# Kernel optimization log

Measured on AMD Instinct MI355X. Metric: run time of the kernel, lower is better.

The kernel has to match this reference:

```python
import jax, jax.numpy as jnp
import numpy as np

EMBED_DIM = 2048
NUM_HEADS = 16
HEAD_DIM = EMBED_DIM // NUM_HEADS
BATCH, SEQ = 4, 4096


def setup_inputs() -> dict:
    key = jax.random.key(0)
    k1, k2, k3, k4 = jax.random.split(key, 4)
    scale = 1.0 / np.sqrt(EMBED_DIM)
    x = jax.random.normal(k1, (BATCH, SEQ, EMBED_DIM), dtype=jnp.float32)
    W_qkv = jax.random.normal(k2, (EMBED_DIM, 3 * EMBED_DIM), dtype=jnp.float32) * scale
    W_out = jax.random.normal(k3, (EMBED_DIM, EMBED_DIM), dtype=jnp.float32) * scale
    b_out = jax.random.normal(k4, (EMBED_DIM,), dtype=jnp.float32) * 0.01
    return {"x": x, "W_qkv": W_qkv, "W_out": W_out, "b_out": b_out}


def reference(x, W_qkv, W_out, b_out):
    b, s, _ = x.shape
    # qkv: (b, s, 3, h, d)
    qkv = (x @ W_qkv).reshape(b, s, 3, NUM_HEADS, HEAD_DIM)
    q, k, v = qkv[:, :, 0], qkv[:, :, 1], qkv[:, :, 2]
    # NOTE: faithful to source — scores mix HEADS per token: (b, s, h, h)
    scores = jnp.einsum('bshd,bsHd->bshH', q, k) / jnp.sqrt(jnp.float32(HEAD_DIM))
    w = jax.nn.softmax(scores, axis=-1)
    attn = jnp.einsum('bshH,bsHd->bshd', w, v).reshape(b, s, EMBED_DIM)
    return attn @ W_out + b_out
```

## Files before the change

kernel.cpp:

```cpp
#include <hip/hip_runtime.h>
#include <hip/hip_bf16.h>
#include <cstdint>


#define TOKENS 16384
#define EMB    2048
#define NQKV   6144

typedef __bf16 bf16x8_t __attribute__((ext_vector_type(8)));
typedef float  f32x4_t  __attribute__((ext_vector_type(4)));

#define GLOAD16(gsrc, ldst)                                                    \
  __builtin_amdgcn_global_load_lds(                                            \
      (const __attribute__((address_space(1))) void*)(uintptr_t)(gsrc),        \
      (__attribute__((address_space(3))) void*)(uint32_t)(uintptr_t)(ldst),    \
      16, 0, 0)

static __device__ __forceinline__ unsigned short f32_to_bf16_bits(float f) {
  union { float f; uint32_t u; } x; x.f = f;
  uint32_t u = x.u;
  u += 0x7fffu + ((u >> 16) & 1u);
  return (unsigned short)(u >> 16);
}

__global__ __launch_bounds__(256) void prep(
    const float4* __restrict__ x4, ushort4* __restrict__ xb4,
    const float* __restrict__ Wqkv, unsigned short* __restrict__ wqkvT,
    const float* __restrict__ Wout, unsigned short* __restrict__ woutT) {
  const int b = blockIdx.x;
  const int t = threadIdx.x;
  if (b < 2048) {
    const int n4 = 33554432 / 4;
    const int stride = 2048 * 256;
    for (int i = b * 256 + t; i < n4; i += stride) {
      float4 v = x4[i];
      ushort4 o;
      o.x = f32_to_bf16_bits(v.x);
      o.y = f32_to_bf16_bits(v.y);
      o.z = f32_to_bf16_bits(v.z);
      o.w = f32_to_bf16_bits(v.w);
      xb4[i] = o;
    }
    return;
  }
  __shared__ float tile[32][33];
  const float* in;
  unsigned short* out;
  int R, C, bxt, byt;
  if (b < 14336) {
    const int bb = b - 2048;
    in = Wqkv; out = wqkvT; R = 2048; C = 6144;
    bxt = bb % 192; byt = bb / 192;
  } else {
    const int bb = b - 14336;
    in = Wout; out = woutT; R = 2048; C = 2048;
    bxt = bb % 64; byt = bb / 64;
  }
  const int bx = bxt * 32;
  const int by = byt * 32;
  const int tx = t & 31;
  const int ty = t >> 5;
#pragma unroll
  for (int j = 0; j < 32; j += 8)
    tile[ty + j][tx] = in[(size_t)(by + ty + j) * C + bx + tx];
  __syncthreads();
#pragma unroll
  for (int j = 0; j < 32; j += 8)
    out[(size_t)(bx + ty + j) * R + by + tx] = f32_to_bf16_bits(tile[tx][ty + j]);
}

template <bool OUT_BF16>
__global__ __launch_bounds__(512, 1) void gemm_bt(
    const unsigned short* __restrict__ A,
    const unsigned short* __restrict__ BT,
    unsigned short* __restrict__ Cb,
    float* __restrict__ Cf,
    const float* __restrict__ bias,
    int M, int N) {
  constexpr int K = 2048;
  constexpr int BK = 64;
  constexpr int NKT = K / BK;
  __shared__ __align__(16) char lds[131072];

  const int nbx = N / 256;
  const int nwg = gridDim.x;
  const int bid = blockIdx.x;
  const int swzb = (bid & 7) * (nwg >> 3) + (bid >> 3);
  const int by = swzb / nbx;
  const int bx = swzb % nbx;

  const int t    = threadIdx.x;
  const int lane = t & 63;
  const int wid  = t >> 6;
  const int wr   = wid >> 2;
  const int wc   = wid & 3;
  const int lr   = lane & 15;
  const int g    = lane >> 4;
  const bool g0  = (wr == 0);

  const unsigned short* aSrc = A  + (size_t)by * 256 * K;
  const unsigned short* bSrc = BT + (size_t)bx * 256 * K;

  int aoff[2], boff[2];
#pragma unroll
  for (int i = 0; i < 2; ++i) {
    const int p   = (i * 512 + t) * 16;
    const int lo  = p ^ (((p >> 7) & 7) << 4);
    const int rih = lo >> 7;
    const int kbe = (lo & 127) >> 1;
    aoff[i] = (((rih >> 6) << 7) + (rih & 63)) * K + kbe;
    boff[i] = (((rih >> 5) << 6) + (rih & 31)) * K + kbe;
  }
  const int ldst = wid << 10;

  auto stageA = [&](int h, int k0, char* bufA) {
#pragma unroll
    for (int i = 0; i < 2; ++i)
      GLOAD16(aSrc + aoff[i] + h * (64 * K) + k0, bufA + h * 16384 + i * 8192 + ldst);
  };
  auto stageB = [&](int h, int k0, char* bufB) {
#pragma unroll
    for (int i = 0; i < 2; ++i)
      GLOAD16(bSrc + boff[i] + h * (32 * K) + k0, bufB + h * 16384 + i * 8192 + ldst);
  };

  const int sw   = (lr & 7) << 4;
  const int col0 = (g * 16) ^ sw;
  const int col1 = (64 + g * 16) ^ sw;
  const int aRow = (wr * 64 + lr) * 128;
  const int bRow = (wc * 32 + lr) * 128;

  f32x4_t acc[8][4] = {};
  bf16x8_t av[4][2];
  bf16x8_t bv0[2][2], bv1[2][2];

#define LDA_INTO(dst, bufA_, q)                                                \
  {                                                                            \
    const char* _b = (bufA_) + (q) * 16384 + aRow;                             \
    _Pragma("unroll") for (int m2 = 0; m2 < 4; ++m2) {                         \
      dst[m2][0] = *(const bf16x8_t*)(_b + m2 * 2048 + col0);                  \
      dst[m2][1] = *(const bf16x8_t*)(_b + m2 * 2048 + col1);                  \
    }                                                                          \
  }
#define LDB_INTO(dst, bufB_, pair)                                             \
  {                                                                            \
    _Pragma("unroll") for (int e = 0; e < 2; ++e) {                            \
      const int nf = (pair) * 2 + e;                                           \
      const char* _b = (bufB_) + (nf >> 1) * 16384 + (nf & 1) * 2048 + bRow;   \
      dst[e][0] = *(const bf16x8_t*)(_b + col0);                               \
      dst[e][1] = *(const bf16x8_t*)(_b + col1);                               \
    }                                                                          \
  }
#define MFMAQ(AV, BV, Q, PAIR)                                                 \
  _Pragma("unroll") for (int m2 = 0; m2 < 4; ++m2)                             \
  _Pragma("unroll") for (int e = 0; e < 2; ++e)                                \
  _Pragma("unroll") for (int ks = 0; ks < 2; ++ks)                             \
    acc[(Q) * 4 + m2][(PAIR) * 2 + e] = __builtin_amdgcn_mfma_f32_16x16x32_bf16( \
        AV[m2][ks], BV[e][ks], acc[(Q) * 4 + m2][(PAIR) * 2 + e], 0, 0, 0);

#define SBR __builtin_amdgcn_sched_barrier(0)
#define BARR __builtin_amdgcn_s_barrier()
#define LGKM0 asm volatile("s_waitcnt lgkmcnt(0)" ::: "memory"); SBR;
#define P1_ __builtin_amdgcn_s_setprio(1);
#define P0_ __builtin_amdgcn_s_setprio(0); SBR;

#define MQ0 { LGKM0; P1_; MFMAQ(av, bv0, 0, 0); MFMAQ(av, bv1, 0, 1); P0_; }
#define MQ1 { LGKM0; P1_; MFMAQ(av, bv0, 1, 0); MFMAQ(av, bv1, 1, 1); P0_; }

#define BODY(KT, SA1, SB2, VMN, MP)                                            \
  {                                                                            \
    char* cA = lds + ((KT) & 1) * 65536;                                       \
    char* cB = cA + 32768;                                                     \
    char* nA = lds + (((KT) + 1) & 1) * 65536;                                 \
    const int k1 = ((KT) + 1) * BK, k2 = ((KT) + 2) * BK;                      \
               \
    if (g0) { LDA_INTO(av, cA, 0); LDB_INTO(bv0, cB, 0); LDB_INTO(bv1, cB, 1); } \
    SBR;                                                                       \
    if (SA1) { stageA(0, k1, nA); } SBR;                                       \
    if (!g0 && (MP)) MQ1;                                                      \
    SBR; BARR;                                                                 \
                        \
    if (!g0) { LDA_INTO(av, cA, 0); LDB_INTO(bv0, cB, 0); LDB_INTO(bv1, cB, 1); } \
    SBR;                                                                       \
    if (SA1) { stageA(1, k1, nA); } SBR;                                       \
    if (g0) MQ0;                                                               \
    SBR; BARR;                                                                 \
                                         \
    if (g0) { LDA_INTO(av, cA, 1); } SBR;                                      \
    if (!g0) MQ0;                                                              \
    SBR; BARR;                                                                 \
                   \
    if (!g0) { LDA_INTO(av, cA, 1); } SBR;                                     \
    if (SB2) { stageB(0, k2, cB); stageB(1, k2, cB); } SBR;                    \
    asm volatile("s_waitcnt vmcnt(" #VMN ")" ::: "memory"); SBR;               \
    if (g0) MQ1;                                                               \
    SBR; BARR;                                                                 \
  }

  {
    char* b0A = lds;
    char* b0B = lds + 32768;
    char* b1B = lds + 65536 + 32768;
    stageB(0, 0, b0B); stageB(1, 0, b0B);
    stageA(0, 0, b0A);
    stageA(1, 0, b0A);
    stageB(0, BK, b1B); stageB(1, BK, b1B);
    asm volatile("s_waitcnt vmcnt(4)" ::: "memory");
    BARR;
  }

  BODY(0, 1, 1, 4, 0);
  for (int kt = 1; kt < NKT - 2; ++kt) {
    BODY(kt, 1, 1, 4, 1);
  }
  BODY(NKT - 2, 1, 0, 0, 1);
  BODY(NKT - 1, 0, 0, 0, 1);
  if (!g0) MQ1;

  const int rbase = by * 256 + wr * 128 + g * 4;
  const int cbase = bx * 256 + wc * 64 + lr;
#pragma unroll
  for (int m = 0; m < 8; ++m) {
#pragma unroll
    for (int nf = 0; nf < 4; ++nf) {
      const int col = cbase + nf * 16;
#pragma unroll
      for (int j = 0; j < 4; ++j) {
        const size_t off = (size_t)(rbase + (m >> 2) * 64 + (m & 3) * 16 + j) * N + col;
        if constexpr (OUT_BF16) {
          Cb[off] = f32_to_bf16_bits(acc[m][nf][j]);
        } else {
          Cf[off] = acc[m][nf][j] + bias[col];
        }
      }
    }
  }
#undef LDA_INTO
#undef LDB_INTO
#undef MFMAQ
#undef SBR
#undef BARR
#undef LGKM0
#undef P1_
#undef P0_
#undef MQ0
#undef MQ1
#undef BODY
}

__global__ __launch_bounds__(256) void attn_heads(
    const unsigned short* __restrict__ qkv,
    unsigned short* __restrict__ attn) {
  __shared__ __align__(16) unsigned short sQKV[NQKV];
  __shared__ float sW[16][16];

  const int t = threadIdx.x;
  const size_t qbase = (size_t)blockIdx.x * NQKV;

  const uint4* gp = (const uint4*)(qkv + qbase);
  uint4* l = (uint4*)sQKV;
#pragma unroll
  for (int i = 0; i < 3; ++i) {
    const int idx = i * 256 + t;
    int dst = idx;
    if (idx >= 256 && idx < 512) {
      const int r = (idx - 256) >> 4;
      const int c = idx & 15;
      dst = 256 + r * 16 + (c ^ (r & 7));
    }
    l[dst] = gp[idx];
  }
  __syncthreads();

  const int h = t >> 4;
  const int H = t & 15;
  const bf16x8_t* q8 = (const bf16x8_t*)sQKV + h * 16;
  const bf16x8_t* k8 = (const bf16x8_t*)sQKV + 256;
  float s = 0.f;
#pragma unroll
  for (int d8 = 0; d8 < 16; ++d8) {
    bf16x8_t qv = q8[d8];
    bf16x8_t kv = k8[H * 16 + (d8 ^ (H & 7))];
#pragma unroll
    for (int j = 0; j < 8; ++j)
      s = fmaf((float)qv[j], (float)kv[j], s);
  }
  s *= 0.08838834764831843f;

  float mx = s;
#pragma unroll
  for (int o = 8; o; o >>= 1) mx = fmaxf(mx, __shfl_xor(mx, o));
  const float e = __expf(s - mx);
  float sum = e;
#pragma unroll
  for (int o = 8; o; o >>= 1) sum += __shfl_xor(sum, o);
  sW[h][H] = e / sum;
  __syncthreads();

  const int d0c = t & 15;
  const bf16x8_t* v8 = (const bf16x8_t*)sQKV + 512;
  float accv[8] = {};
#pragma unroll
  for (int j = 0; j < 16; ++j) {
    const float w = sW[h][j];
    const bf16x8_t vv = v8[j * 16 + d0c];
#pragma unroll
    for (int jj = 0; jj < 8; ++jj)
      accv[jj] = fmaf(w, (float)vv[jj], accv[jj]);
  }
  bf16x8_t o;
#pragma unroll
  for (int jj = 0; jj < 8; ++jj) o[jj] = (__bf16)accv[jj];
  *(bf16x8_t*)(attn + (size_t)blockIdx.x * EMB + h * 128 + d0c * 8) = o;
}

extern "C" void kernel_launch(void* const* d_in, const int* in_sizes, int n_in,
                              void* d_out, int out_size, void* d_ws, size_t ws_size,
                              hipStream_t stream) {
  const float* x    = (const float*)d_in[0];
  const float* Wqkv = (const float*)d_in[1];
  const float* Wout = (const float*)d_in[2];
  const float* bout = (const float*)d_in[3];
  float* out = (float*)d_out;

  unsigned short* xb    = (unsigned short*)d_ws;
  unsigned short* wqkvT = xb    + (size_t)33554432;
  unsigned short* woutT = wqkvT + (size_t)12582912;
  unsigned short* qkv   = woutT + (size_t)4194304;
  unsigned short* attn  = qkv   + (size_t)100663296;

  prep<<<18432, 256, 0, stream>>>((const float4*)x, (ushort4*)xb,
                                  Wqkv, wqkvT, Wout, woutT);
  gemm_bt<true><<<(16384 / 256) * (6144 / 256), 512, 0, stream>>>(
      xb, wqkvT, qkv, nullptr, nullptr, 16384, 6144);
  attn_heads<<<TOKENS, 256, 0, stream>>>(qkv, attn);
  gemm_bt<false><<<(16384 / 256) * (2048 / 256), 512, 0, stream>>>(
      attn, woutT, nullptr, out, bout, 16384, 2048);
}
```

Baseline: 598.2 us.

## Compute per-token head attention with MFMA, one token per wavefront

Replaces the scalar-FMA per-token head-mixing attention kernel with one that handles one token per wavefront and four tokens per block. QK^T and PV are computed with 16x16x32 bf16 MFMA instructions, softmax runs across lanes with shuffles, and only V is staged in LDS, with a word swizzle to spread banks. The aim is to cut ALU work, LDS traffic and block-sync overhead in the middle stage, at the cost of half-zeroed MFMA operands for PV and scalar 2-byte LDS gathers for V. P is rounded to bf16 before the PV product, which adds a small precision difference.

```diff
diff --git a/kernel.cpp b/kernel.cpp
--- a/kernel.cpp
+++ b/kernel.cpp
@@ -9,6 +9,7 @@
 
 typedef __bf16 bf16x8_t __attribute__((ext_vector_type(8)));
 typedef float  f32x4_t  __attribute__((ext_vector_type(4)));
+typedef unsigned short ushort8_t __attribute__((ext_vector_type(8)));
 
 #define GLOAD16(gsrc, ldst)                                                    \
   __builtin_amdgcn_global_load_lds(                                            \
@@ -21,6 +22,10 @@
   uint32_t u = x.u;
   u += 0x7fffu + ((u >> 16) & 1u);
   return (unsigned short)(u >> 16);
+}
+
+static __device__ __forceinline__ unsigned int pack_bf16(float lo, float hi) {
+  return ((unsigned int)f32_to_bf16_bits(hi) << 16) | (unsigned int)f32_to_bf16_bits(lo);
 }
 
 __global__ __launch_bounds__(256) void prep(
@@ -173,23 +178,19 @@
     char* cB = cA + 32768;                                                     \
     char* nA = lds + (((KT) + 1) & 1) * 65536;                                 \
     const int k1 = ((KT) + 1) * BK, k2 = ((KT) + 2) * BK;                      \
-               \
     if (g0) { LDA_INTO(av, cA, 0); LDB_INTO(bv0, cB, 0); LDB_INTO(bv1, cB, 1); } \
     SBR;                                                                       \
     if (SA1) { stageA(0, k1, nA); } SBR;                                       \
     if (!g0 && (MP)) MQ1;                                                      \
     SBR; BARR;                                                                 \
-                        \
     if (!g0) { LDA_INTO(av, cA, 0); LDB_INTO(bv0, cB, 0); LDB_INTO(bv1, cB, 1); } \
     SBR;                                                                       \
     if (SA1) { stageA(1, k1, nA); } SBR;                                       \
     if (g0) MQ0;                                                               \
     SBR; BARR;                                                                 \
-                                         \
     if (g0) { LDA_INTO(av, cA, 1); } SBR;                                      \
     if (!g0) MQ0;                                                              \
     SBR; BARR;                                                                 \
-                   \
     if (!g0) { LDA_INTO(av, cA, 1); } SBR;                                     \
     if (SB2) { stageB(0, k2, cB); stageB(1, k2, cB); } SBR;                    \
     asm volatile("s_waitcnt vmcnt(" #VMN ")" ::: "memory"); SBR;               \
@@ -248,70 +249,92 @@
 #undef BODY
 }
 
-__global__ __launch_bounds__(256) void attn_heads(
+__global__ __launch_bounds__(256) void attn_mfma(
     const unsigned short* __restrict__ qkv,
     unsigned short* __restrict__ attn) {
-  __shared__ __align__(16) unsigned short sQKV[NQKV];
-  __shared__ float sW[16][16];
-
-  const int t = threadIdx.x;
-  const size_t qbase = (size_t)blockIdx.x * NQKV;
-
-  const uint4* gp = (const uint4*)(qkv + qbase);
-  uint4* l = (uint4*)sQKV;
-#pragma unroll
-  for (int i = 0; i < 3; ++i) {
-    const int idx = i * 256 + t;
-    int dst = idx;
-    if (idx >= 256 && idx < 512) {
-      const int r = (idx - 256) >> 4;
-      const int c = idx & 15;
-      dst = 256 + r * 16 + (c ^ (r & 7));
+  __shared__ __align__(16) unsigned short sV[4][2048];
+
+  const int t  = threadIdx.x;
+  const int w  = t >> 6;
+  const int l  = t & 63;
+  const int lr = l & 15;
+  const int g  = l >> 4;
+  const size_t tok = (size_t)blockIdx.x * 4 + w;
+  const unsigned short* base = qkv + tok * NQKV;
+
+  {
+    const uint4* vg = (const uint4*)(base + 4096);
+    uint4* vl = (uint4*)&sV[w][0];
+#pragma unroll
+    for (int i = 0; i < 4; ++i) {
+      const int idx = i * 64 + l;
+      uint4 v = vg[idx];
+      if (idx & 128) {
+        uint4 o; o.x = v.y; o.y = v.x; o.z = v.w; o.w = v.z;
+        vl[idx] = o;
+      } else {
+        vl[idx] = v;
+      }
     }
-    l[dst] = gp[idx];
-  }
-  __syncthreads();
-
-  const int h = t >> 4;
-  const int H = t & 15;
-  const bf16x8_t* q8 = (const bf16x8_t*)sQKV + h * 16;
-  const bf16x8_t* k8 = (const bf16x8_t*)sQKV + 256;
-  float s = 0.f;
-#pragma unroll
-  for (int d8 = 0; d8 < 16; ++d8) {
-    bf16x8_t qv = q8[d8];
-    bf16x8_t kv = k8[H * 16 + (d8 ^ (H & 7))];
-#pragma unroll
-    for (int j = 0; j < 8; ++j)
-      s = fmaf((float)qv[j], (float)kv[j], s);
-  }
-  s *= 0.08838834764831843f;
-
-  float mx = s;
-#pragma unroll
-  for (int o = 8; o; o >>= 1) mx = fmaxf(mx, __shfl_xor(mx, o));
-  const float e = __expf(s - mx);
-  float sum = e;
-#pragma unroll
-  for (int o = 8; o; o >>= 1) sum += __shfl_xor(sum, o);
-  sW[h][H] = e / sum;
-  __syncthreads();
-
-  const int d0c = t & 15;
-  const bf16x8_t* v8 = (const bf16x8_t*)sQKV + 512;
-  float accv[8] = {};
-#pragma unroll
-  for (int j = 0; j < 16; ++j) {
-    const float w = sW[h][j];
-    const bf16x8_t vv = v8[j * 16 + d0c];
-#pragma unroll
-    for (int jj = 0; jj < 8; ++jj)
-      accv[jj] = fmaf(w, (float)vv[jj], accv[jj]);
-  }
-  bf16x8_t o;
-#pragma unroll
-  for (int jj = 0; jj < 8; ++jj) o[jj] = (__bf16)accv[jj];
-  *(bf16x8_t*)(attn + (size_t)blockIdx.x * EMB + h * 128 + d0c * 8) = o;
+  }
+
+  f32x4_t s = {};
+#pragma unroll
+  for (int ch = 0; ch < 4; ++ch) {
+    bf16x8_t ka = *(const bf16x8_t*)(base + 2048 + lr * 128 + ch * 32 + g * 8);
+    bf16x8_t qb = *(const bf16x8_t*)(base +        lr * 128 + ch * 32 + g * 8);
+    s = __builtin_amdgcn_mfma_f32_16x16x32_bf16(ka, qb, s, 0, 0, 0);
+  }
+
+  float p0 = s[0] * 0.08838834764831843f;
+  float p1 = s[1] * 0.08838834764831843f;
+  float p2 = s[2] * 0.08838834764831843f;
+  float p3 = s[3] * 0.08838834764831843f;
+  float mx = fmaxf(fmaxf(p0, p1), fmaxf(p2, p3));
+  mx = fmaxf(mx, __shfl_xor(mx, 16));
+  mx = fmaxf(mx, __shfl_xor(mx, 32));
+  p0 = __expf(p0 - mx);
+  p1 = __expf(p1 - mx);
+  p2 = __expf(p2 - mx);
+  p3 = __expf(p3 - mx);
+  float sum = p0 + p1 + p2 + p3;
+  sum += __shfl_xor(sum, 16);
+  sum += __shfl_xor(sum, 32);
+  const float inv = 1.0f / sum;
+
+  const unsigned int u01 = pack_bf16(p0, p1);
+  const unsigned int u23 = pack_bf16(p2, p3);
+  const int gs = (g & 1) * 2;
+  const int m1 = (gs << 4) | lr;
+  const int m2 = m1 + 16;
+  union { uint4 u; bf16x8_t b; } pB;
+  pB.u.x = __shfl(u01, m1);
+  pB.u.y = __shfl(u23, m1);
+  pB.u.z = __shfl(u01, m2);
+  pB.u.w = __shfl(u23, m2);
+  if (g >= 2) { pB.u.x = 0; pB.u.y = 0; pB.u.z = 0; pB.u.w = 0; }
+
+  const char* vbase = (const char*)&sV[w][0];
+  const int dbyte = (lr * 2) ^ (g < 2 ? (g << 2) : 0);
+#pragma unroll
+  for (int ch = 0; ch < 8; ++ch) {
+    union { ushort8_t u; bf16x8_t b; } va;
+    if (g < 2) {
+#pragma unroll
+      for (int j = 0; j < 8; ++j) {
+        const int H = g * 8 + j;
+        va.u[j] = *(const unsigned short*)(vbase + H * 256 + ch * 32 + dbyte);
+      }
+    } else {
+      va.u = (ushort8_t){0, 0, 0, 0, 0, 0, 0, 0};
+    }
+    f32x4_t z = {};
+    f32x4_t o = __builtin_amdgcn_mfma_f32_16x16x32_bf16(va.b, pB.b, z, 0, 0, 0);
+    uint2 st;
+    st.x = pack_bf16(o[0] * inv, o[1] * inv);
+    st.y = pack_bf16(o[2] * inv, o[3] * inv);
+    *(uint2*)(attn + tok * EMB + lr * 128 + ch * 16 + g * 4) = st;
+  }
 }
 
 extern "C" void kernel_launch(void* const* d_in, const int* in_sizes, int n_in,
@@ -333,7 +356,7 @@
                                   Wqkv, wqkvT, Wout, woutT);
   gemm_bt<true><<<(16384 / 256) * (6144 / 256), 512, 0, stream>>>(
       xb, wqkvT, qkv, nullptr, nullptr, 16384, 6144);
-  attn_heads<<<TOKENS, 256, 0, stream>>>(qkv, attn);
+  attn_mfma<<<TOKENS / 4, 256, 0, stream>>>(qkv, attn);
   gemm_bt<false><<<(16384 / 256) * (2048 / 256), 512, 0, stream>>>(
       attn, woutT, nullptr, out, bout, 16384, 2048);
 }
```

After: 583.1 us. 1.03x faster.
